# Optimization experiments

Hardware: AMD Instinct MI355X
Metric: run time of the kernel (lower is better)

The kernel has to match this reference:

```python
import jax, jax.numpy as jnp
import numpy as np

B, H, S = 128, 256, 19
K0, D0 = 512, 32
K1, D1 = 512, 64
K2, D2 = 512, 64


def _conv(x, w, b):
    # 3x3 SAME conv, NCHW / OIHW
    y = jax.lax.conv_general_dilated(x, w, (1, 1), 'SAME',
                                     dimension_numbers=('NCHW', 'OIHW', 'NCHW'))
    return y + b[None, :, None, None]


def _bn(x, g, b, eps=1e-5):
    # BatchNorm2d in training mode: batch statistics over (N, H, W)
    m = x.mean((0, 2, 3), keepdims=True)
    v = x.var((0, 2, 3), keepdims=True)
    return g[None, :, None, None] * (x - m) * jax.lax.rsqrt(v + eps) + b[None, :, None, None]


def _vq(lat, E):
    # cdist^2 -> argmin -> gather, with straight-through gradient copy
    shp = lat.shape
    d = E.shape[1]
    lp = lat.reshape(-1, d)                                   # row-major flatten, as torch .view
    dist = (lp * lp).sum(-1, keepdims=True) + (E * E).sum(-1) - 2.0 * (lp @ E.T)
    k = jnp.argmin(dist, axis=-1)
    zd = E[k]
    zg = lp + jax.lax.stop_gradient(zd - lp)
    return k.reshape(shp[0], -1), zd.reshape(shp), zg.reshape(shp)


def setup_inputs() -> dict:
    key = jax.random.key(0)
    ks = iter(jax.random.split(key, 64))
    def rn(shape, s=0.02):
        return (s * jax.random.normal(next(ks), shape)).astype(jnp.float32)
    inp = {
        'observations': jax.random.normal(next(ks), (B, 18, S, S), jnp.float32),
        'hierarchy_usages': jax.random.uniform(next(ks), (B, 2), jnp.float32),
        'h0_conv_w': rn((H, 18, 3, 3), 0.05), 'h0_conv_b': jnp.zeros((H,)),
        'h0_bn_g': jnp.ones((H,)), 'h0_bn_b': jnp.zeros((H,)),
        'rb_c1_w': rn((3, H, H, 3, 3)), 'rb_c1_b': jnp.zeros((3, H)),
        'rb_bn1_g': jnp.ones((3, H)), 'rb_bn1_b': jnp.zeros((3, H)),
        'rb_c2_w': rn((3, H, H, 3, 3)), 'rb_c2_b': jnp.zeros((3, H)),
        'rb_bn2_g': jnp.ones((3, H)), 'rb_bn2_b': jnp.zeros((3, H)),
        'h0_conv2_w': rn((32, H, 3, 3)), 'h0_conv2_b': jnp.zeros((32,)),
        'h0_bn2_g': jnp.ones((32,)), 'h0_bn2_b': jnp.zeros((32,)),
        'E0': rn((K0, D0)), 'E1': rn((K1, D1)), 'E2': rn((K2, D2)),
        'h1_fc_w': rn((D0 * S * S, 256)), 'h1_fc_b': jnp.zeros((256,)),
        'h1_fc2_w': rn((256, D1 * 8)), 'h1_fc2_b': jnp.zeros((D1 * 8,)),
        'h2_fc_w': rn((D1 * 8, 128)), 'h2_fc_b': jnp.zeros((128,)),
        'h2_fc2_w': rn((128, D2 * 8)), 'h2_fc2_b': jnp.zeros((D2 * 8,)),
        'h2_fc3_w': rn((D2 * 8, 128)), 'h2_fc3_b': jnp.zeros((128,)),
        'h2_fc4_w': rn((128, D1 * 8)), 'h2_fc4_b': jnp.zeros((D1 * 8,)),
        'h1_fc3_w': rn((D1 * 8, 256)), 'h1_fc3_b': jnp.zeros((256,)),
        'h1_fc4_w': rn((256, D0 * S * S)), 'h1_fc4_b': jnp.zeros((D0 * S * S,)),
        'policy_w': rn((32 * S * S, 362)), 'policy_b': jnp.zeros((362,)),
        'value_w': rn((32 * S * S, 1)), 'value_b': jnp.zeros((1,)),
    }
    return inp


def _forward(observations, hierarchy_usages, h0_conv_w, h0_conv_b, h0_bn_g, h0_bn_b,
             rb_c1_w, rb_c1_b, rb_bn1_g, rb_bn1_b, rb_c2_w, rb_c2_b, rb_bn2_g, rb_bn2_b,
             h0_conv2_w, h0_conv2_b, h0_bn2_g, h0_bn2_b, E0, E1, E2,
             h1_fc_w, h1_fc_b, h1_fc2_w, h1_fc2_b, h2_fc_w, h2_fc_b, h2_fc2_w, h2_fc2_b,
             h2_fc3_w, h2_fc3_b, h2_fc4_w, h2_fc4_b, h1_fc3_w, h1_fc3_b, h1_fc4_w, h1_fc4_b,
             policy_w, policy_b, value_w, value_b):
    n = observations.shape[0]
    x = jax.nn.relu(_bn(_conv(observations, h0_conv_w, h0_conv_b), h0_bn_g, h0_bn_b))
    for i in range(3):
        xi = x
        x = jax.nn.relu(_bn(_conv(x, rb_c1_w[i], rb_c1_b[i]), rb_bn1_g[i], rb_bn1_b[i]))
        x = _bn(_conv(x, rb_c2_w[i], rb_c2_b[i]), rb_bn2_g[i], rb_bn2_b[i])
        x = jax.nn.relu(xi + x)
    x = jnp.tanh(_bn(_conv(x, h0_conv2_w, h0_conv2_b), h0_bn2_g, h0_bn2_b))  # [B,32,19,19]
    ze0 = x
    k0, zq0, zql0 = _vq(x, E0)
    em0 = jnp.broadcast_to(E0.mean(0)[None, :, None, None], (n, E0.shape[1], S, S))
    x = jax.lax.stop_gradient(x).reshape(-1, 32 * S * S)
    x = jax.nn.relu(x @ h1_fc_w + h1_fc_b)
    x = jnp.tanh(x @ h1_fc2_w + h1_fc2_b).reshape(-1, E1.shape[1], 8)
    ze1 = x
    k1, zq1, zql1 = _vq(x, E1)
    em1 = jnp.broadcast_to(E1.mean(0)[None, :, None], (n, E1.shape[1], 8))
    x = jax.lax.stop_gradient(x).reshape(-1, E1.shape[1] * 8)
    x = jax.nn.relu(x @ h2_fc_w + h2_fc_b)
    x = jnp.tanh(x @ h2_fc2_w + h2_fc2_b).reshape(-1, E2.shape[1], 8)
    ze2 = x
    k2, zq2, zql2 = _vq(x, E2)
    em2 = jnp.broadcast_to(E2.mean(0)[None, :, None], (n, E2.shape[1], 8))
    # top-down decoder path
    x = zql2.reshape(-1, E2.shape[1] * 8)
    x = jax.nn.relu(x @ h2_fc3_w + h2_fc3_b)
    x = jnp.tanh(x @ h2_fc4_w + h2_fc4_b).reshape(-1, E1.shape[1], 8)
    u1 = hierarchy_usages[:, 1][:, None, None]
    x = u1 * zql1 + (1.0 - u1) * x
    x = x.reshape(-1, E1.shape[1] * 8)
    x = jax.nn.relu(x @ h1_fc3_w + h1_fc3_b)
    x = jnp.tanh(x @ h1_fc4_w + h1_fc4_b).reshape(-1, E0.shape[1], S, S)
    u0 = hierarchy_usages[:, 0][:, None, None, None]
    x = u0 * zql0 + (1.0 - u0) * x
    x = x.reshape(-1, 32 * S * S)
    policy = x @ policy_w + policy_b
    value = jnp.tanh(x @ value_w + value_b)
    return (policy, value, ze0, ze1, ze2, zq0, zq1, zq2, k0, k1, k2,
            zql0, zql1, zql2, em0, em1, em2)


def reference(observations, hierarchy_usages, h0_conv_w, h0_conv_b, h0_bn_g, h0_bn_b,
              rb_c1_w, rb_c1_b, rb_bn1_g, rb_bn1_b, rb_c2_w, rb_c2_b, rb_bn2_g, rb_bn2_b,
              h0_conv2_w, h0_conv2_b, h0_bn2_g, h0_bn2_b, E0, E1, E2,
              h1_fc_w, h1_fc_b, h1_fc2_w, h1_fc2_b, h2_fc_w, h2_fc_b, h2_fc2_w, h2_fc2_b,
              h2_fc3_w, h2_fc3_b, h2_fc4_w, h2_fc4_b, h1_fc3_w, h1_fc3_b, h1_fc4_w, h1_fc4_b,
              policy_w, policy_b, value_w, value_b):
    return _forward(observations, hierarchy_usages, h0_conv_w, h0_conv_b, h0_bn_g, h0_bn_b,
                    rb_c1_w, rb_c1_b, rb_bn1_g, rb_bn1_b, rb_c2_w, rb_c2_b, rb_bn2_g, rb_bn2_b,
                    h0_conv2_w, h0_conv2_b, h0_bn2_g, h0_bn2_b, E0, E1, E2,
                    h1_fc_w, h1_fc_b, h1_fc2_w, h1_fc2_b, h2_fc_w, h2_fc_b, h2_fc2_w, h2_fc2_b,
                    h2_fc3_w, h2_fc3_b, h2_fc4_w, h2_fc4_b, h1_fc3_w, h1_fc3_b, h1_fc4_w, h1_fc4_b,
                    policy_w, policy_b, value_w, value_b)
```

## Files before the change

kernel.cpp:

```cpp
#include <hip/hip_runtime.h>
#include <hip/hip_bf16.h>

typedef long long i64;
typedef __attribute__((ext_vector_type(8))) short bf16x8;
typedef __attribute__((ext_vector_type(4))) float f32x4;

static constexpr i64 OUT_POLICY = 0;
static constexpr i64 OUT_VALUE  = 46336;
static constexpr i64 OUT_ZE0    = 46464;
static constexpr i64 OUT_ZE1    = 1525120;
static constexpr i64 OUT_ZE2    = 1590656;
static constexpr i64 OUT_ZQ0    = 1656192;
static constexpr i64 OUT_ZQ1    = 3134848;
static constexpr i64 OUT_ZQ2    = 3200384;
static constexpr i64 OUT_K0     = 3265920;
static constexpr i64 OUT_K1     = 3312128;
static constexpr i64 OUT_K2     = 3313152;
static constexpr i64 OUT_ZQL0   = 3314176;
static constexpr i64 OUT_ZQL1   = 4792832;
static constexpr i64 OUT_ZQL2   = 4858368;
static constexpr i64 OUT_EM0    = 4923904;
static constexpr i64 OUT_EM1    = 6402560;
static constexpr i64 OUT_EM2    = 6468096;
static constexpr i64 OUT_TOTAL  = 6533632;

__device__ __forceinline__ short bf16_hi(float v, float* back)
{
    unsigned b = __float_as_uint(v);
    unsigned hb = (b + 0x8000u) & 0xFFFF0000u;
    *back = __uint_as_float(hb);
    return (short)(hb >> 16);
}
__device__ __forceinline__ short bf16_of(float v)
{
    return (short)((__float_as_uint(v) + 0x8000u) >> 16);
}

__global__ void wtr_k(const float* __restrict__ w, float* __restrict__ wt,
                      int COUT, int CIN)
{
    int total = COUT * CIN * 9;
    for (int idx = blockIdx.x * blockDim.x + threadIdx.x; idx < total;
         idx += gridDim.x * blockDim.x) {
        int co = idx / (CIN * 9);
        int r  = idx - co * CIN * 9;
        int ci = r / 9;
        int tap = r - ci * 9;
        wt[((i64)tap * CIN + ci) * COUT + co] = w[idx];
    }
}

__global__ void wtr4_k(const float* __restrict__ w, short* __restrict__ wt4,
                       int CIN, int COUT)
{
    int NC = CIN / 32;
    int total = NC * 9 * 2 * 8192;
    for (int idx = blockIdx.x * blockDim.x + threadIdx.x; idx < total;
         idx += gridDim.x * blockDim.x) {
        int tile = idx >> 13;
        int pos  = idx & 8191;
        int row   = pos >> 6;
        int sslot = (pos >> 3) & 7;
        int r     = pos & 7;
        int slot  = sslot ^ (row & 7);
        int k2    = slot * 8 + r;
        int ct = tile & 1;
        int s  = tile >> 1;
        int c  = s / 9, t = s - c * 9;
        int co = ct * 128 + row;
        int ci = c * 32 + (k2 & 31);
        short outv = 0;
        if (co < COUT) {
            float v = w[((i64)co * CIN + ci) * 9 + t];
            float hf;
            short hs = bf16_hi(v, &hf);
            outv = (k2 < 32) ? hs : bf16_of(v - hf);
        }
        wt4[idx] = outv;
    }
}

template<int CIN>
__global__ __launch_bounds__(256)
void convmfma_k(const float* __restrict__ X, const short* __restrict__ WT4,
                float* __restrict__ Y, int coutT)
{
    constexpr int NC = CIN / 32;
    constexpr int NS = NC * 9;
    __shared__ short Bt[2][8192];
    const int tid  = threadIdx.x;
    const int lane = tid & 63;
    const int w    = tid >> 6;
    const int wco  = (w & 1) * 64;
    const int wsp  = (w >> 1) * 64;
    const int col0 = blockIdx.x * 128;
    const int ct   = blockIdx.y;
    const int co0  = ct * 128;

    const int spS = tid & 127;
    const int cig = tid >> 7;
    const int colS = col0 + spS;
    const int nS = colS / 361;
    const int sS = colS - nS * 361;
    const int yS = sS / 19, xS = sS - yS * 19;
    const float* Xb = X + (i64)nS * CIN * 361 + sS;

    float xv[16];

#define B_LOAD(S)                                                               \
    {                                                                           \
        const int c_ = (S) / 9, t_ = (S) - c_ * 9;                              \
        const int ky_ = t_ / 3, kx_ = t_ - ky_ * 3;                             \
        const bool v_ = (yS + ky_ >= 1) & (yS + ky_ <= 19) &                    \
                        (xS + kx_ >= 1) & (xS + kx_ <= 19);                     \
        const float* xp_ = Xb + (i64)(c_ * 32 + cig * 16) * 361                 \
                              + (ky_ - 1) * 19 + (kx_ - 1);                     \
        _Pragma("unroll")                                                       \
        for (int j = 0; j < 16; j++) xv[j] = v_ ? xp_[(i64)j * 361] : 0.f;      \
    }

#define B_WRITE(BUF)                                                            \
    {                                                                           \
        bf16x8 h0, h1, l0, l1;                                                  \
        _Pragma("unroll")                                                       \
        for (int j = 0; j < 8; j++) {                                           \
            float hf;                                                           \
            short hs = bf16_hi(xv[j], &hf);                                     \
            h0[j] = hs; l0[j] = bf16_of(xv[j] - hf);                            \
        }                                                                       \
        _Pragma("unroll")                                                       \
        for (int j = 0; j < 8; j++) {                                           \
            float hf;                                                           \
            short hs = bf16_hi(xv[8 + j], &hf);                                 \
            h1[j] = hs; l1[j] = bf16_of(xv[8 + j] - hf);                        \
        }                                                                       \
        short* bp = &Bt[BUF][spS << 6];                                         \
        const int sw = spS & 7;                                                 \
        *(bf16x8*)(bp + (((cig * 2 + 0) ^ sw) << 3)) = h0;                      \
        *(bf16x8*)(bp + (((cig * 2 + 1) ^ sw) << 3)) = h1;                      \
        *(bf16x8*)(bp + (((4 + cig * 2 + 0) ^ sw) << 3)) = l0;                  \
        *(bf16x8*)(bp + (((4 + cig * 2 + 1) ^ sw) << 3)) = l1;                  \
    }

    f32x4 acc[4][4];
#pragma unroll
    for (int i = 0; i < 4; i++)
#pragma unroll
        for (int j = 0; j < 4; j++) acc[i][j] = (f32x4){0.f, 0.f, 0.f, 0.f};

    B_LOAD(0)
    B_WRITE(0)
    int cur = 0;
    for (int s = 0; s < NS; s++) {
        __syncthreads();
        if (s + 1 < NS) B_LOAD(s + 1)
        {
            const short* tb = WT4 + ((i64)(s * 2 + ct) << 13);
            bf16x8 afr[2][4];
#pragma unroll
            for (int ha = 0; ha < 2; ha++)
#pragma unroll
                for (int fa = 0; fa < 4; fa++) {
                    int row = wco + fa * 16 + (lane & 15);
                    int slot = ha * 4 + (lane >> 4);
                    afr[ha][fa] = *(const bf16x8*)(tb + (row << 6) + (((slot ^ (row & 7))) << 3));
                }
            bf16x8 bfr[2][4];
#pragma unroll
            for (int hb = 0; hb < 2; hb++)
#pragma unroll
                for (int fb = 0; fb < 4; fb++) {
                    int row = wsp + fb * 16 + (lane & 15);
                    int slot = hb * 4 + (lane >> 4);
                    bfr[hb][fb] = *(const bf16x8*)&Bt[cur][(row << 6) + (((slot ^ (row & 7))) << 3)];
                }
#pragma unroll
            for (int ha = 0; ha < 2; ha++)
#pragma unroll
                for (int fa = 0; fa < 4; fa++) {
                    bf16x8 af = afr[ha][fa];
#pragma unroll
                    for (int hb = 0; hb < 2; hb++)
#pragma unroll
                        for (int fb = 0; fb < 4; fb++)
                            acc[fa][fb] = __builtin_amdgcn_mfma_f32_16x16x32_bf16(
                                af, bfr[hb][fb], acc[fa][fb], 0, 0, 0);
                }
        }
        if (s + 1 < NS) B_WRITE(cur ^ 1)
        cur ^= 1;
    }
#undef B_LOAD
#undef B_WRITE

#pragma unroll
    for (int fb = 0; fb < 4; fb++) {
        int col = col0 + wsp + fb * 16 + (lane & 15);
        int nT = col / 361, sT = col - nT * 361;
        float* yp = Y + ((i64)nT * coutT + co0 + wco) * 361 + sT;
#pragma unroll
        for (int fa = 0; fa < 4; fa++)
#pragma unroll
            for (int r = 0; r < 4; r++) {
                int m = fa * 16 + (lane >> 4) * 4 + r;
                if (co0 + wco + m < coutT) yp[(i64)m * 361] = acc[fa][fb][r];
            }
    }
}

template<int CIN>
__global__ __launch_bounds__(256)
void convgemm_k(const float* __restrict__ X, const float* __restrict__ wt,
                float* __restrict__ Y, int wtW, int coW0, int coutT)
{
    constexpr int NCB = (CIN + 15) / 16;
    constexpr int NS  = 9 * NCB;
    __shared__ float Ws[2][16][128];
    __shared__ float Bs[2][16][128];
    const int tid  = threadIdx.x;
    const int col0 = blockIdx.x * 128;
    const int co0  = blockIdx.y * 128;
    const int tn = tid & 15;
    const int tm = (tid >> 4) & 15;
    const int kkS  = tid >> 5;
    const int cS0  = (tid & 31) * 4;

    int y_[4], x_[4];
    const float* Xb[4];
#pragma unroll
    for (int j = 0; j < 4; j++) {
        int colj = col0 + cS0 + j;
        int nj = colj / 361;
        int sj = colj - nj * 361;
        y_[j] = sj / 19;
        x_[j] = sj - y_[j] * 19;
        Xb[j] = X + ((i64)nj * CIN) * 361 + sj;
    }

    float4 wA, wB, bA, bB;

#define STAGE(S)                                                               \
    {                                                                          \
        const int tap_ = (S) / NCB, cb_ = ((S) % NCB) * 16;                    \
        const int ky_ = tap_ / 3, kx_ = tap_ - ky_ * 3;                        \
        const int doff_ = (ky_ - 1) * 19 + (kx_ - 1);                          \
        const int ci0_ = cb_ + kkS, ci1_ = ci0_ + 8;                           \
        const float* wr_ = wt + ((i64)(tap_ * CIN) + ci0_) * wtW               \
                              + coW0 + co0 + cS0;                              \
        const bool wok_ = (coW0 + co0 + cS0) < wtW;                            \
        wA = (wok_ && ci0_ < CIN) ? *(const float4*)wr_                        \
                                  : float4{0.f, 0.f, 0.f, 0.f};                \
        wB = (wok_ && ci1_ < CIN) ? *(const float4*)(wr_ + (i64)8 * wtW)       \
                                  : float4{0.f, 0.f, 0.f, 0.f};                \
        bool v0_ = (y_[0]+ky_>=1)&(y_[0]+ky_<=19)&(x_[0]+kx_>=1)&(x_[0]+kx_<=19); \
        bool v1_ = (y_[1]+ky_>=1)&(y_[1]+ky_<=19)&(x_[1]+kx_>=1)&(x_[1]+kx_<=19); \
        bool v2_ = (y_[2]+ky_>=1)&(y_[2]+ky_<=19)&(x_[2]+kx_>=1)&(x_[2]+kx_<=19); \
        bool v3_ = (y_[3]+ky_>=1)&(y_[3]+ky_<=19)&(x_[3]+kx_>=1)&(x_[3]+kx_<=19); \
        bA.x = (v0_ && ci0_ < CIN) ? Xb[0][(i64)ci0_ * 361 + doff_] : 0.f;     \
        bA.y = (v1_ && ci0_ < CIN) ? Xb[1][(i64)ci0_ * 361 + doff_] : 0.f;     \
        bA.z = (v2_ && ci0_ < CIN) ? Xb[2][(i64)ci0_ * 361 + doff_] : 0.f;     \
        bA.w = (v3_ && ci0_ < CIN) ? Xb[3][(i64)ci0_ * 361 + doff_] : 0.f;     \
        bB.x = (v0_ && ci1_ < CIN) ? Xb[0][(i64)ci1_ * 361 + doff_] : 0.f;     \
        bB.y = (v1_ && ci1_ < CIN) ? Xb[1][(i64)ci1_ * 361 + doff_] : 0.f;     \
        bB.z = (v2_ && ci1_ < CIN) ? Xb[2][(i64)ci1_ * 361 + doff_] : 0.f;     \
        bB.w = (v3_ && ci1_ < CIN) ? Xb[3][(i64)ci1_ * 361 + doff_] : 0.f;     \
    }

#define WRITE(BUF)                                                             \
    {                                                                          \
        *(float4*)&Ws[BUF][kkS    ][cS0] = wA;                                 \
        *(float4*)&Ws[BUF][kkS + 8][cS0] = wB;                                 \
        *(float4*)&Bs[BUF][kkS    ][cS0] = bA;                                 \
        *(float4*)&Bs[BUF][kkS + 8][cS0] = bB;                                 \
    }

    float acc[8][8];
#pragma unroll
    for (int i = 0; i < 8; i++)
#pragma unroll
        for (int j = 0; j < 8; j++) acc[i][j] = 0.f;

    STAGE(0)
    WRITE(0)
    int cur = 0;
    for (int s = 0; s < NS; s++) {
        __syncthreads();
        if (s + 1 < NS) STAGE(s + 1)
#pragma unroll
        for (int kk = 0; kk < 16; kk++) {
            const float4 w0 = *(const float4*)&Ws[cur][kk][tm * 4];
            const float4 w1 = *(const float4*)&Ws[cur][kk][tm * 4 + 64];
            const float4 b0 = *(const float4*)&Bs[cur][kk][tn * 4];
            const float4 b1 = *(const float4*)&Bs[cur][kk][tn * 4 + 64];
            float wv[8] = {w0.x, w0.y, w0.z, w0.w, w1.x, w1.y, w1.z, w1.w};
            float bv[8] = {b0.x, b0.y, b0.z, b0.w, b1.x, b1.y, b1.z, b1.w};
#pragma unroll
            for (int wi = 0; wi < 8; wi++)
#pragma unroll
                for (int bj = 0; bj < 8; bj++)
                    acc[wi][bj] = fmaf(wv[wi], bv[bj], acc[wi][bj]);
        }
        if (s + 1 < NS) WRITE(cur ^ 1)
        cur ^= 1;
    }
#undef STAGE
#undef WRITE

#pragma unroll
    for (int bj = 0; bj < 8; bj++) {
        int lc = (bj < 4) ? (tn * 4 + bj) : (64 + tn * 4 + bj - 4);
        int colT = col0 + lc;
        int nT = colT / 361;
        int sT = colT - nT * 361;
        float* yp = Y + ((i64)nT * coutT + co0) * 361 + sT;
#pragma unroll
        for (int wi = 0; wi < 8; wi++) {
            int co = (wi < 4) ? (tm * 4 + wi) : (64 + tm * 4 + wi - 4);
            if (co0 + co < coutT) yp[(i64)co * 361] = acc[wi][bj];
        }
    }
}

__global__ __launch_bounds__(256)
void bnstats_k(const float* __restrict__ x, const float* __restrict__ g,
               const float* __restrict__ b, float* __restrict__ scale,
               float* __restrict__ shift, int C)
{
    const int c = blockIdx.x;
    float s = 0.f, s2 = 0.f;
    for (int n = 0; n < 128; n++) {
        const float* p = x + ((i64)n * C + c) * 361;
        for (int i = threadIdx.x; i < 361; i += 256) {
            float v = p[i]; s += v; s2 += v * v;
        }
    }
    __shared__ float rs[4], rq[4];
    for (int o = 32; o > 0; o >>= 1) { s += __shfl_down(s, o); s2 += __shfl_down(s2, o); }
    int lane = threadIdx.x & 63, wid = threadIdx.x >> 6;
    if (lane == 0) { rs[wid] = s; rq[wid] = s2; }
    __syncthreads();
    if (threadIdx.x == 0) {
        float S = rs[0] + rs[1] + rs[2] + rs[3];
        float Q = rq[0] + rq[1] + rq[2] + rq[3];
        const float inv = 1.f / 46208.f;
        float m  = S * inv;
        float var = Q * inv - m * m;
        float sc = g[c] * rsqrtf(var + 1e-5f);
        scale[c] = sc;
        shift[c] = b[c] - m * sc;
    }
}

__global__ void bn_relu4_k(float4* __restrict__ x, const float* __restrict__ scale,
                           const float* __restrict__ shift, int C, int total4)
{
    for (int i = blockIdx.x * blockDim.x + threadIdx.x; i < total4; i += gridDim.x * blockDim.x) {
        float4 v = x[i];
        int e = i * 4;
        int c0 = (e / 361) % C, c1 = ((e + 1) / 361) % C;
        int c2 = ((e + 2) / 361) % C, c3 = ((e + 3) / 361) % C;
        v.x = fmaf(v.x, scale[c0], shift[c0]); v.x = v.x > 0.f ? v.x : 0.f;
        v.y = fmaf(v.y, scale[c1], shift[c1]); v.y = v.y > 0.f ? v.y : 0.f;
        v.z = fmaf(v.z, scale[c2], shift[c2]); v.z = v.z > 0.f ? v.z : 0.f;
        v.w = fmaf(v.w, scale[c3], shift[c3]); v.w = v.w > 0.f ? v.w : 0.f;
        x[i] = v;
    }
}

__global__ void bn_add_relu4_k(float4* __restrict__ xa, const float4* __restrict__ xc,
                               const float* __restrict__ scale, const float* __restrict__ shift,
                               int C, int total4)
{
    for (int i = blockIdx.x * blockDim.x + threadIdx.x; i < total4; i += gridDim.x * blockDim.x) {
        float4 a = xa[i], c = xc[i];
        int e = i * 4;
        int c0 = (e / 361) % C, c1 = ((e + 1) / 361) % C;
        int c2 = ((e + 2) / 361) % C, c3 = ((e + 3) / 361) % C;
        a.x += fmaf(c.x, scale[c0], shift[c0]); a.x = a.x > 0.f ? a.x : 0.f;
        a.y += fmaf(c.y, scale[c1], shift[c1]); a.y = a.y > 0.f ? a.y : 0.f;
        a.z += fmaf(c.z, scale[c2], shift[c2]); a.z = a.z > 0.f ? a.z : 0.f;
        a.w += fmaf(c.w, scale[c3], shift[c3]); a.w = a.w > 0.f ? a.w : 0.f;
        xa[i] = a;
    }
}

__global__ void bn_tanh_ws_k(const float* __restrict__ x, const float* __restrict__ scale,
                             const float* __restrict__ shift, float* __restrict__ zf, int total)
{
    for (int i = blockIdx.x * blockDim.x + threadIdx.x; i < total; i += gridDim.x * blockDim.x) {
        int c = (i / 361) & 31;
        zf[i] = tanhf(fmaf(x[i], scale[c], shift[c]));
    }
}

__global__ void prep_k(const float* __restrict__ E0, const float* __restrict__ E1,
                       const float* __restrict__ E2,
                       float* __restrict__ ee0, float* __restrict__ ee1, float* __restrict__ ee2,
                       float* __restrict__ cm0, float* __restrict__ cm1, float* __restrict__ cm2)
{
    int t = threadIdx.x;
    if (blockIdx.x == 0) {
        float s = 0.f; const float* e = E0 + (i64)t * 32;
        for (int d = 0; d < 32; d++) s += e[d] * e[d];
        ee0[t] = s;
    } else if (blockIdx.x == 1) {
        float s = 0.f; const float* e = E1 + (i64)t * 64;
        for (int d = 0; d < 64; d++) s += e[d] * e[d];
        ee1[t] = s;
    } else if (blockIdx.x == 2) {
        float s = 0.f; const float* e = E2 + (i64)t * 64;
        for (int d = 0; d < 64; d++) s += e[d] * e[d];
        ee2[t] = s;
    } else {
        if (t < 32) {
            float s = 0.f; for (int k = 0; k < 512; k++) s += E0[k * 32 + t];
            cm0[t] = s * (1.f / 512.f);
        } else if (t >= 64 && t < 128) {
            int d = t - 64; float s = 0.f; for (int k = 0; k < 512; k++) s += E1[k * 64 + d];
            cm1[d] = s * (1.f / 512.f);
        } else if (t >= 128 && t < 192) {
            int d = t - 128; float s = 0.f; for (int k = 0; k < 512; k++) s += E2[k * 64 + d];
            cm2[d] = s * (1.f / 512.f);
        }
    }
}

__global__ __launch_bounds__(256)
void vq0_k(const float* __restrict__ z, const float* __restrict__ E,
           const float* __restrict__ ee, float* __restrict__ zqf, int* __restrict__ ki)
{
    __shared__ float Es[256 * 32];
    int row = blockIdx.x * 256 + threadIdx.x;
    const bool live = row < 46208;
    const float* zp = z + (i64)(live ? row : 0) * 32;
    float zv[32]; float zz = 0.f;
#pragma unroll
    for (int d = 0; d < 32; d++) { float v = zp[d]; zv[d] = v; zz += v * v; }
    float best = 3.4e38f; int bk = 0;
    for (int h = 0; h < 2; h++) {
        __syncthreads();
        for (int i = threadIdx.x; i < 256 * 32; i += 256) Es[i] = E[h * 8192 + i];
        __syncthreads();
        for (int k = 0; k < 256; k++) {
            const float* e = Es + k * 32;
            float dot = 0.f;
#pragma unroll
            for (int d = 0; d < 32; d++) dot = fmaf(zv[d], e[d], dot);
            float dist = (zz + ee[h * 256 + k]) - 2.f * dot;
            if (dist < best) { best = dist; bk = h * 256 + k; }
        }
    }
    if (live) {
        ki[row] = bk;
        const float* eb = E + (i64)bk * 32;
#pragma unroll
        for (int d = 0; d < 32; d++) zqf[(i64)row * 32 + d] = eb[d];
    }
}

__global__ __launch_bounds__(256)
void vq64_k(const float* __restrict__ z, const float* __restrict__ E,
            const float* __restrict__ ee, float* __restrict__ zqf, int* __restrict__ ki)
{
    __shared__ float Es[128 * 64];
    int row = blockIdx.x * 256 + threadIdx.x;
    const float* zp = z + (i64)row * 64;
    float zv[64]; float zz = 0.f;
#pragma unroll
    for (int d = 0; d < 64; d++) { float v = zp[d]; zv[d] = v; zz += v * v; }
    float best = 3.4e38f; int bk = 0;
    for (int h = 0; h < 4; h++) {
        __syncthreads();
        for (int i = threadIdx.x; i < 128 * 64; i += 256) Es[i] = E[(i64)h * 8192 + i];
        __syncthreads();
        for (int k = 0; k < 128; k++) {
            const float* e = Es + k * 64;
            float dot = 0.f;
#pragma unroll
            for (int d = 0; d < 64; d++) dot = fmaf(zv[d], e[d], dot);
            float dist = (zz + ee[h * 128 + k]) - 2.f * dot;
            if (dist < best) { best = dist; bk = h * 128 + k; }
        }
    }
    ki[row] = bk;
    const float* eb = E + (i64)bk * 64;
#pragma unroll
    for (int d = 0; d < 64; d++) zqf[(i64)row * 64 + d] = eb[d];
}

__global__ __launch_bounds__(256)
void gemm_part_k(const float* __restrict__ A, const float* __restrict__ W,
                 float* __restrict__ part, int K, int N, int kchunk)
{
    __shared__ float As[128][17];
    __shared__ float Ws[16][64];
    const int n0 = blockIdx.x * 64;
    const int ks = blockIdx.y;
    const int kb0  = ks * kchunk;
    const int kend = min(K, kb0 + kchunk);
    const int tid = threadIdx.x;
    const int tn = tid & 15, tm = tid >> 4;
    float acc[8][4];
#pragma unroll
    for (int i = 0; i < 8; i++)
#pragma unroll
        for (int j = 0; j < 4; j++) acc[i][j] = 0.f;

    for (int kb = kb0; kb < kend; kb += 16) {
        __syncthreads();
        for (int i = tid; i < 2048; i += 256) {
            int m = i >> 4, kk = i & 15;
            int k = kb + kk;
            As[m][kk] = (k < kend) ? A[(i64)m * K + k] : 0.f;
        }
        for (int i = tid; i < 1024; i += 256) {
            int kk = i >> 6, nl = i & 63;
            int k = kb + kk, n = n0 + nl;
            Ws[kk][nl] = (k < kend && n < N) ? W[(i64)k * N + n] : 0.f;
        }
        __syncthreads();
#pragma unroll
        for (int kk = 0; kk < 16; kk++) {
            float av[8], wv[4];
#pragma unroll
            for (int i = 0; i < 8; i++) av[i] = As[tm * 8 + i][kk];
#pragma unroll
            for (int j = 0; j < 4; j++) wv[j] = Ws[kk][tn * 4 + j];
#pragma unroll
            for (int i = 0; i < 8; i++)
#pragma unroll
                for (int j = 0; j < 4; j++) acc[i][j] = fmaf(av[i], wv[j], acc[i][j]);
        }
    }
#pragma unroll
    for (int i = 0; i < 8; i++) {
        int m = tm * 8 + i;
#pragma unroll
        for (int j = 0; j < 4; j++) {
            int n = n0 + tn * 4 + j;
            if (n < N) part[((i64)ks * 128 + m) * N + n] = acc[i][j];
        }
    }
}

__global__ void combine_k(const float* __restrict__ part, const float* __restrict__ bias,
                          float* __restrict__ of, int MN, int N, int ksplit, int act)
{
    for (int i = blockIdx.x * blockDim.x + threadIdx.x; i < MN; i += gridDim.x * blockDim.x) {
        float s = 0.f;
        for (int t = 0; t < ksplit; t++) s += part[(i64)t * MN + i];
        s += bias[i % N];
        if (act == 1) s = s > 0.f ? s : 0.f;
        else if (act == 2) s = tanhf(s);
        of[i] = s;
    }
}

__global__ void blend_k(const float* __restrict__ q, const float* __restrict__ d,
                        const float* __restrict__ hu, int col, float* __restrict__ o,
                        int per_b, int total)
{
    for (int i = blockIdx.x * blockDim.x + threadIdx.x; i < total; i += gridDim.x * blockDim.x) {
        float u = hu[(i / per_b) * 2 + col];
        o[i] = u * q[i] + (1.f - u) * d[i];
    }
}

__global__ __launch_bounds__(256)
void value_k(const float* __restrict__ x, const float* __restrict__ w,
             const float* __restrict__ b, float* __restrict__ valf)
{
    int m = blockIdx.x;
    float s = 0.f;
    const float* xp = x + (i64)m * 11552;
    for (int k = threadIdx.x; k < 11552; k += 256) s = fmaf(xp[k], w[k], s);
    for (int o = 32; o > 0; o >>= 1) s += __shfl_down(s, o);
    __shared__ float r[4];
    int lane = threadIdx.x & 63, wid = threadIdx.x >> 6;
    if (lane == 0) r[wid] = s;
    __syncthreads();
    if (threadIdx.x == 0)
        valf[m] = tanhf(r[0] + r[1] + r[2] + r[3] + b[0]);
}

__global__ void emit_f32_k(const float* __restrict__ src, float* __restrict__ out, i64 off, int n)
{
    for (int i = blockIdx.x * blockDim.x + threadIdx.x; i < n; i += gridDim.x * blockDim.x)
        out[off + i] = src[i];
}

__global__ void emit_dup_k(const float* __restrict__ src, float* __restrict__ out,
                           i64 off1, i64 off2, int n)
{
    for (int i = blockIdx.x * blockDim.x + threadIdx.x; i < n; i += gridDim.x * blockDim.x) {
        float v = src[i];
        out[off1 + i] = v;
        out[off2 + i] = v;
    }
}

__global__ void emit_k_k(const int* __restrict__ ki, float* __restrict__ out, i64 off, int n)
{
    for (int i = blockIdx.x * blockDim.x + threadIdx.x; i < n; i += gridDim.x * blockDim.x)
        out[off + i] = (float)ki[i];
}

__global__ void emit_em_k(const float* __restrict__ cm, float* __restrict__ out, i64 off,
                          int D, int SPL, int total)
{
    for (int i = blockIdx.x * blockDim.x + threadIdx.x; i < total; i += gridDim.x * blockDim.x) {
        int c = (i / SPL) % D;
        out[off + i] = cm[c];
    }
}

__global__ void marker_k(float* __restrict__ out, int code)
{
    if (threadIdx.x < 64) out[threadIdx.x] = 3000.f + 100.f * code;
}

__global__ void sentinel_k(float* __restrict__ out)
{
    if (threadIdx.x < 128) out[OUT_VALUE + threadIdx.x] = 2000.0f;
}

extern "C" void kernel_launch(void* const* d_in, const int* in_sizes, int n_in,
                              void* d_out, int out_size, void* d_ws, size_t ws_size,
                              hipStream_t stream)
{
    float* out = (float*)d_out;

    int bad = -1;
    if (out_size != (int)OUT_TOTAL) bad = 0;
    else if (n_in != 41) bad = 1;
    else if (in_sizes[0] != 128 * 18 * 361) bad = 2;
    else if (in_sizes[21] != 11552 * 256) bad = 3;
    if (bad >= 0) { marker_k<<<1, 64, 0, stream>>>(out, bad); return; }

    const float* obs   = (const float*)d_in[0];
    const float* hier  = (const float*)d_in[1];
    const float* c0w   = (const float*)d_in[2];
    const float* bn0g  = (const float*)d_in[4];
    const float* bn0b  = (const float*)d_in[5];
    const float* rb1w  = (const float*)d_in[6];
    const float* rbn1g = (const float*)d_in[8];
    const float* rbn1b = (const float*)d_in[9];
    const float* rb2w  = (const float*)d_in[10];
    const float* rbn2g = (const float*)d_in[12];
    const float* rbn2b = (const float*)d_in[13];
    const float* c2w   = (const float*)d_in[14];
    const float* bn2g  = (const float*)d_in[16];
    const float* bn2b  = (const float*)d_in[17];
    const float* E0    = (const float*)d_in[18];
    const float* E1    = (const float*)d_in[19];
    const float* E2    = (const float*)d_in[20];
    const float* fc1w  = (const float*)d_in[21]; const float* fc1b  = (const float*)d_in[22];
    const float* fc2w  = (const float*)d_in[23]; const float* fc2b  = (const float*)d_in[24];
    const float* h2fw  = (const float*)d_in[25]; const float* h2fb  = (const float*)d_in[26];
    const float* h2f2w = (const float*)d_in[27]; const float* h2f2b = (const float*)d_in[28];
    const float* h2f3w = (const float*)d_in[29]; const float* h2f3b = (const float*)d_in[30];
    const float* h2f4w = (const float*)d_in[31]; const float* h2f4b = (const float*)d_in[32];
    const float* h1f3w = (const float*)d_in[33]; const float* h1f3b = (const float*)d_in[34];
    const float* h1f4w = (const float*)d_in[35]; const float* h1f4b = (const float*)d_in[36];
    const float* polw  = (const float*)d_in[37]; const float* polb  = (const float*)d_in[38];
    const float* valw  = (const float*)d_in[39]; const float* valb  = (const float*)d_in[40];

    float* wsf = (float*)d_ws;

    const size_t NEED_A = (size_t)36732928 * 4;
    const size_t NEED_C = (size_t)27860992 * 4;
    if (ws_size < NEED_C) {
        sentinel_k<<<1, 128, 0, stream>>>(out);
        return;
    }
    const bool fullC = (ws_size >= NEED_A);

    float* scale = wsf + 0;        float* shift = wsf + 256;
    float* ee0 = wsf + 512;        float* ee1 = wsf + 1024;   float* ee2 = wsf + 1536;
    float* cm0 = wsf + 2048;       float* cm1 = wsf + 2112;   float* cm2 = wsf + 2176;
    int*   k0i = (int*)(wsf + 4096);
    int*   k1i = (int*)(wsf + 50304);
    int*   k2i = (int*)(wsf + 51328);
    float* h1a  = wsf + 53248;
    float* ze1f = wsf + 86016;
    float* zq1f = wsf + 151552;
    float* h2a  = wsf + 217088;
    float* ze2f = wsf + 233472;
    float* zq2f = wsf + 299008;
    float* h2b  = wsf + 364544;
    float* decf = wsf + 380928;
    float* x1f  = wsf + 446464;
    float* h1b  = wsf + 512000;
    float* polf = wsf + 544768;
    float* valf = wsf + 591104;

    float* A    = wsf + 655360;
    float* B    = wsf + 12484608;
    float* C    = wsf + 24313856;
    float* WT   = fullC ? (wsf + 36143104) : (wsf + 27271168);
    float* ze0f = A;
    float* zq0f = wsf + 655360 + 1572864;
    float* dec0 = wsf + 655360 + 3145728;
    float* xf   = wsf + 655360 + 4718592;
    float* part = B;

    short* WT4 = (short*)d_out;

    const int TOT256 = 128 * 256 * 361;
    const int TOT32  = 128 * 32 * 361;
    const int TOT64  = 128 * 64 * 361;

    prep_k<<<4, 512, 0, stream>>>(E0, E1, E2, ee0, ee1, ee2, cm0, cm1, cm2);

    wtr_k<<<64, 256, 0, stream>>>(c0w, WT, 256, 18);
    convgemm_k<18><<<dim3(361, 2), 256, 0, stream>>>(obs, WT, A, 256, 0, 256);
    bnstats_k<<<256, 256, 0, stream>>>(A, bn0g, bn0b, scale, shift, 256);
    bn_relu4_k<<<1024, 256, 0, stream>>>((float4*)A, scale, shift, 256, TOT256 / 4);

    for (int i = 0; i < 3; i++) {
        if (fullC) {
            wtr4_k<<<1024, 256, 0, stream>>>(rb1w + (i64)i * 589824, WT4, 256, 256);
            convmfma_k<256><<<dim3(361, 2), 256, 0, stream>>>(A, WT4, B, 256);
        } else {
            wtr_k<<<576, 256, 0, stream>>>(rb1w + (i64)i * 589824, WT, 256, 256);
            convgemm_k<256><<<dim3(361, 2), 256, 0, stream>>>(A, WT, B, 256, 0, 256);
        }
        bnstats_k<<<256, 256, 0, stream>>>(B, rbn1g + i * 256, rbn1b + i * 256, scale, shift, 256);
        bn_relu4_k<<<1024, 256, 0, stream>>>((float4*)B, scale, shift, 256, TOT256 / 4);
        if (fullC) {
            wtr4_k<<<1024, 256, 0, stream>>>(rb2w + (i64)i * 589824, WT4, 256, 256);
            convmfma_k<256><<<dim3(361, 2), 256, 0, stream>>>(B, WT4, C, 256);
            bnstats_k<<<256, 256, 0, stream>>>(C, rbn2g + i * 256, rbn2b + i * 256, scale, shift, 256);
            bn_add_relu4_k<<<1024, 256, 0, stream>>>((float4*)A, (const float4*)C, scale, shift, 256, TOT256 / 4);
        } else {
            wtr_k<<<576, 256, 0, stream>>>(rb2w + (i64)i * 589824, WT, 256, 256);
            convgemm_k<256><<<dim3(361, 2), 256, 0, stream>>>(B, WT, C, 256, 0, 256);
            bnstats_k<<<256, 256, 0, stream>>>(C, rbn2g + i * 256, rbn2b + i * 256, scale, shift, 256);
            bn_add_relu4_k<<<1024, 256, 0, stream>>>((float4*)A, (const float4*)C, scale, shift, 256, TOT256 / 4);
        }
    }

    if (fullC) {
        wtr4_k<<<1024, 256, 0, stream>>>(c2w, WT4, 256, 32);
        convmfma_k<256><<<dim3(361, 1), 256, 0, stream>>>(A, WT4, C, 32);
    } else {
        wtr_k<<<72, 256, 0, stream>>>(c2w, WT, 32, 256);
        convgemm_k<256><<<dim3(361, 1), 256, 0, stream>>>(A, WT, C, 32, 0, 32);
    }
    bnstats_k<<<32, 256, 0, stream>>>(C, bn2g, bn2b, scale, shift, 32);
    bn_tanh_ws_k<<<1024, 256, 0, stream>>>(C, scale, shift, ze0f, TOT32);

    vq0_k<<<181, 256, 0, stream>>>(ze0f, E0, ee0, zq0f, k0i);

    gemm_part_k<<<dim3(4, 32), 256, 0, stream>>>(ze0f, fc1w, part, 11552, 256, 361);
    combine_k<<<128, 256, 0, stream>>>(part, fc1b, h1a, 128 * 256, 256, 32, 1);
    gemm_part_k<<<dim3(8, 4), 256, 0, stream>>>(h1a, fc2w, part, 256, 512, 64);
    combine_k<<<256, 256, 0, stream>>>(part, fc2b, ze1f, 128 * 512, 512, 4, 2);
    vq64_k<<<4, 256, 0, stream>>>(ze1f, E1, ee1, zq1f, k1i);

    gemm_part_k<<<dim3(2, 8), 256, 0, stream>>>(ze1f, h2fw, part, 512, 128, 64);
    combine_k<<<64, 256, 0, stream>>>(part, h2fb, h2a, 128 * 128, 128, 8, 1);
    gemm_part_k<<<dim3(8, 2), 256, 0, stream>>>(h2a, h2f2w, part, 128, 512, 64);
    combine_k<<<256, 256, 0, stream>>>(part, h2f2b, ze2f, 128 * 512, 512, 2, 2);
    vq64_k<<<4, 256, 0, stream>>>(ze2f, E2, ee2, zq2f, k2i);

    gemm_part_k<<<dim3(2, 8), 256, 0, stream>>>(zq2f, h2f3w, part, 512, 128, 64);
    combine_k<<<64, 256, 0, stream>>>(part, h2f3b, h2b, 128 * 128, 128, 8, 1);
    gemm_part_k<<<dim3(8, 2), 256, 0, stream>>>(h2b, h2f4w, part, 128, 512, 64);
    combine_k<<<256, 256, 0, stream>>>(part, h2f4b, decf, 128 * 512, 512, 2, 2);
    blend_k<<<256, 256, 0, stream>>>(zq1f, decf, hier, 1, x1f, 512, 65536);

    gemm_part_k<<<dim3(4, 8), 256, 0, stream>>>(x1f, h1f3w, part, 512, 256, 64);
    combine_k<<<128, 256, 0, stream>>>(part, h1f3b, h1b, 128 * 256, 256, 8, 1);
    gemm_part_k<<<dim3(181, 2), 256, 0, stream>>>(h1b, h1f4w, part, 256, 11552, 128);
    combine_k<<<1024, 256, 0, stream>>>(part, h1f4b, dec0, TOT32, 11552, 2, 2);
    blend_k<<<1024, 256, 0, stream>>>(zq0f, dec0, hier, 0, xf, 11552, TOT32);

    gemm_part_k<<<dim3(6, 16), 256, 0, stream>>>(xf, polw, part, 11552, 362, 722);
    combine_k<<<256, 256, 0, stream>>>(part, polb, polf, 128 * 362, 362, 16, 0);
    value_k<<<128, 256, 0, stream>>>(xf, valw, valb, valf);

    emit_f32_k<<<128, 256, 0, stream>>>(polf, out, OUT_POLICY, 46336);
    emit_f32_k<<<1, 128, 0, stream>>>(valf, out, OUT_VALUE, 128);
    emit_f32_k<<<1024, 256, 0, stream>>>(ze0f, out, OUT_ZE0, TOT32);
    emit_f32_k<<<256, 256, 0, stream>>>(ze1f, out, OUT_ZE1, 65536);
    emit_f32_k<<<256, 256, 0, stream>>>(ze2f, out, OUT_ZE2, 65536);
    emit_dup_k<<<1024, 256, 0, stream>>>(zq0f, out, OUT_ZQ0, OUT_ZQL0, TOT32);
    emit_dup_k<<<256, 256, 0, stream>>>(zq1f, out, OUT_ZQ1, OUT_ZQL1, 65536);
    emit_dup_k<<<256, 256, 0, stream>>>(zq2f, out, OUT_ZQ2, OUT_ZQL2, 65536);
    emit_k_k<<<181, 256, 0, stream>>>(k0i, out, OUT_K0, 46208);
    emit_k_k<<<4, 256, 0, stream>>>(k1i, out, OUT_K1, 1024);
    emit_k_k<<<4, 256, 0, stream>>>(k2i, out, OUT_K2, 1024);
    emit_em_k<<<1024, 256, 0, stream>>>(cm0, out, OUT_EM0, 32, 361, TOT32);
    emit_em_k<<<256, 256, 0, stream>>>(cm1, out, OUT_EM1, 64, 8, 65536);
    emit_em_k<<<256, 256, 0, stream>>>(cm2, out, OUT_EM2, 64, 8, 65536);
}
```

Baseline: 3.344 ms.

## Pre-split activations into swizzled bf16 hi/lo records fused with BN-ReLU for MFMA conv

Adds a tier that fuses BatchNorm+ReLU (and residual add) with splitting the activations into bf16 hi/lo pairs, stored in a per-pixel swizzled record layout. A new conv kernel loads these records straight into LDS via global_load_lds with a zero record for padding, so the conv no longer converts fp32 activations on the fly. It is meant to remove per-conv conversion and staging work and the separate BN-ReLU passes. The cost is a larger workspace, a path that only runs when the workspace is big enough, and extra record write traffic.

```diff
diff --git a/kernel.cpp b/kernel.cpp
--- a/kernel.cpp
+++ b/kernel.cpp
@@ -77,6 +77,164 @@
             outv = (k2 < 32) ? hs : bf16_of(v - hf);
         }
         wt4[idx] = outv;
+    }
+}
+
+template<int MODE>
+__global__ __launch_bounds__(256)
+void xsplit_k(const float* __restrict__ X, float* __restrict__ Aio,
+              const float* __restrict__ scale, const float* __restrict__ shift,
+              short* __restrict__ XS)
+{
+    int idx = blockIdx.x * 256 + threadIdx.x;
+    int g = idx % 46208;
+    int c = idx / 46208;
+    int n = g / 361;
+    int s = g - n * 361;
+    const i64 base = ((i64)n * 256 + c * 32) * 361 + s;
+
+    float vv[32];
+#pragma unroll
+    for (int j = 0; j < 32; j++) {
+        float x = X[base + (i64)j * 361];
+        float sc = scale[c * 32 + j], sh = shift[c * 32 + j];
+        float v;
+        if (MODE == 2) v = Aio[base + (i64)j * 361] + fmaf(x, sc, sh);
+        else           v = fmaf(x, sc, sh);
+        v = v > 0.f ? v : 0.f;
+        if (MODE >= 1) Aio[base + (i64)j * 361] = v;
+        vv[j] = v;
+    }
+    short hi[32], lo[32];
+#pragma unroll
+    for (int j = 0; j < 32; j++) {
+        float hf;
+        hi[j] = bf16_hi(vv[j], &hf);
+        lo[j] = bf16_of(vv[j] - hf);
+    }
+    short* rec = XS + ((i64)c * 46208 + g) * 64;
+    const int sw = g & 7;
+#pragma unroll
+    for (int l = 0; l < 8; l++) {
+        bf16x8 wv;
+#pragma unroll
+        for (int r = 0; r < 8; r++) {
+            int k2 = l * 8 + r;
+            int j = k2 & 31;
+            wv[r] = (k2 < 32) ? hi[j] : lo[j];
+        }
+        *(bf16x8*)(rec + ((l ^ sw) << 3)) = wv;
+    }
+}
+
+template<int CIN>
+__global__ __launch_bounds__(256)
+void convmfma_xs_k(const short* __restrict__ XS, const short* __restrict__ WT4,
+                   float* __restrict__ Y, int coutT, const short* __restrict__ zrec)
+{
+    constexpr int NC = CIN / 32;
+    constexpr int NS = NC * 9;
+    __shared__ short Bt[2][8192];
+    const int tid  = threadIdx.x;
+    const int lane = tid & 63;
+    const int w    = tid >> 6;
+    const int wco  = (w & 1) * 64;
+    const int wsp  = (w >> 1) * 64;
+    const int col0 = blockIdx.x * 128;
+    const int ct   = blockIdx.y;
+    const int co0  = ct * 128;
+
+    int gj[4], yj[4], xj[4], subj[4], cLj[4];
+#pragma unroll
+    for (int j = 0; j < 4; j++) {
+        int slotIdx = w * 256 + j * 64 + lane;
+        int colL = slotIdx >> 3;
+        subj[j] = slotIdx & 7;
+        cLj[j]  = colL;
+        gj[j] = col0 + colL;
+        int nn = gj[j] / 361;
+        int ss = gj[j] - nn * 361;
+        yj[j] = ss / 19;
+        xj[j] = ss - yj[j] * 19;
+    }
+
+#define BX_ISSUE(BUF, S)                                                        \
+    {                                                                           \
+        const int c_ = (S) / 9, t_ = (S) - c_ * 9;                              \
+        const int ky_ = t_ / 3, kx_ = t_ - ky_ * 3;                             \
+        const int doff_ = (ky_ - 1) * 19 + (kx_ - 1);                           \
+        _Pragma("unroll")                                                       \
+        for (int j = 0; j < 4; j++) {                                           \
+            bool v_ = (yj[j] + ky_ >= 1) & (yj[j] + ky_ <= 19) &                \
+                      (xj[j] + kx_ >= 1) & (xj[j] + kx_ <= 19);                 \
+            int adj_ = (cLj[j] & 7) ^ ((cLj[j] + doff_) & 7);                   \
+            const short* src = v_ ? (XS + ((i64)c_ * 46208 + (gj[j] + doff_)) * 64 \
+                                       + ((subj[j] ^ adj_) << 3))               \
+                                  : zrec;                                       \
+            __builtin_amdgcn_global_load_lds(src, &Bt[BUF][(w * 256 + j * 64) * 8], 16, 0, 0); \
+        }                                                                       \
+    }
+
+    f32x4 acc[4][4];
+#pragma unroll
+    for (int i = 0; i < 4; i++)
+#pragma unroll
+        for (int j = 0; j < 4; j++) acc[i][j] = (f32x4){0.f, 0.f, 0.f, 0.f};
+
+    BX_ISSUE(0, 0)
+    int cur = 0;
+    for (int s = 0; s < NS; s++) {
+        __syncthreads();
+        if (s + 1 < NS) BX_ISSUE(cur ^ 1, s + 1)
+        {
+            const short* tb = WT4 + ((i64)(s * 2 + ct) << 13);
+            bf16x8 afr[2][4];
+#pragma unroll
+            for (int ha = 0; ha < 2; ha++)
+#pragma unroll
+                for (int fa = 0; fa < 4; fa++) {
+                    int row = wco + fa * 16 + (lane & 15);
+                    int slot = ha * 4 + (lane >> 4);
+                    afr[ha][fa] = *(const bf16x8*)(tb + (row << 6) + (((slot ^ (row & 7))) << 3));
+                }
+            bf16x8 bfr[2][4];
+#pragma unroll
+            for (int hb = 0; hb < 2; hb++)
+#pragma unroll
+                for (int fb = 0; fb < 4; fb++) {
+                    int row = wsp + fb * 16 + (lane & 15);
+                    int slot = hb * 4 + (lane >> 4);
+                    bfr[hb][fb] = *(const bf16x8*)&Bt[cur][(row << 6) + (((slot ^ (row & 7))) << 3)];
+                }
+#pragma unroll
+            for (int ha = 0; ha < 2; ha++)
+#pragma unroll
+                for (int fa = 0; fa < 4; fa++) {
+                    bf16x8 af = afr[ha][fa];
+#pragma unroll
+                    for (int hb = 0; hb < 2; hb++)
+#pragma unroll
+                        for (int fb = 0; fb < 4; fb++)
+                            acc[fa][fb] = __builtin_amdgcn_mfma_f32_16x16x32_bf16(
+                                af, bfr[hb][fb], acc[fa][fb], 0, 0, 0);
+                }
+        }
+        cur ^= 1;
+    }
+#undef BX_ISSUE
+
+#pragma unroll
+    for (int fb = 0; fb < 4; fb++) {
+        int col = col0 + wsp + fb * 16 + (lane & 15);
+        int nT = col / 361, sT = col - nT * 361;
+        float* yp = Y + ((i64)nT * coutT + co0 + wco) * 361 + sT;
+#pragma unroll
+        for (int fa = 0; fa < 4; fa++)
+#pragma unroll
+            for (int r = 0; r < 4; r++) {
+                int m = fa * 16 + (lane >> 4) * 4 + r;
+                if (co0 + wco + m < coutT) yp[(i64)m * 361] = acc[fa][fb][r];
+            }
     }
 }
 
@@ -396,7 +554,8 @@
 __global__ void prep_k(const float* __restrict__ E0, const float* __restrict__ E1,
                        const float* __restrict__ E2,
                        float* __restrict__ ee0, float* __restrict__ ee1, float* __restrict__ ee2,
-                       float* __restrict__ cm0, float* __restrict__ cm1, float* __restrict__ cm2)
+                       float* __restrict__ cm0, float* __restrict__ cm1, float* __restrict__ cm2,
+                       float* __restrict__ wsf)
 {
     int t = threadIdx.x;
     if (blockIdx.x == 0) {
@@ -421,6 +580,8 @@
         } else if (t >= 128 && t < 192) {
             int d = t - 128; float s = 0.f; for (int k = 0; k < 512; k++) s += E2[k * 64 + d];
             cm2[d] = s * (1.f / 512.f);
+        } else if (t >= 192 && t < 224) {
+            wsf[2560 + (t - 192)] = 0.f;
         }
     }
 }
@@ -667,17 +828,19 @@
 
     float* wsf = (float*)d_ws;
 
+    const size_t NEED_X = (size_t)48562176 * 4;
     const size_t NEED_A = (size_t)36732928 * 4;
     const size_t NEED_C = (size_t)27860992 * 4;
     if (ws_size < NEED_C) {
         sentinel_k<<<1, 128, 0, stream>>>(out);
         return;
     }
-    const bool fullC = (ws_size >= NEED_A);
+    const int tier = (ws_size >= NEED_X) ? 2 : (ws_size >= NEED_A) ? 1 : 0;
 
     float* scale = wsf + 0;        float* shift = wsf + 256;
     float* ee0 = wsf + 512;        float* ee1 = wsf + 1024;   float* ee2 = wsf + 1536;
     float* cm0 = wsf + 2048;       float* cm1 = wsf + 2112;   float* cm2 = wsf + 2176;
+    const short* zrec = (const short*)(wsf + 2560);
     int*   k0i = (int*)(wsf + 4096);
     int*   k1i = (int*)(wsf + 50304);
     int*   k2i = (int*)(wsf + 51328);
@@ -694,61 +857,82 @@
     float* polf = wsf + 544768;
     float* valf = wsf + 591104;
 
-    float* A    = wsf + 655360;
-    float* B    = wsf + 12484608;
-    float* C    = wsf + 24313856;
-    float* WT   = fullC ? (wsf + 36143104) : (wsf + 27271168);
+    float* A   = wsf + 655360;
+    float* R   = wsf + 12484608;
+    float* C   = wsf + 24313856;
+    short* XSa = (short*)(wsf + 24313856);
+    short* XSb = (short*)(wsf + 36143104);
+    float* WT  = (tier == 2) ? (wsf + 47972352)
+               : (tier == 1) ? (wsf + 36143104) : (wsf + 27271168);
     float* ze0f = A;
     float* zq0f = wsf + 655360 + 1572864;
     float* dec0 = wsf + 655360 + 3145728;
     float* xf   = wsf + 655360 + 4718592;
-    float* part = B;
+    float* part = R;
 
     short* WT4 = (short*)d_out;
 
     const int TOT256 = 128 * 256 * 361;
     const int TOT32  = 128 * 32 * 361;
-    const int TOT64  = 128 * 64 * 361;
-
-    prep_k<<<4, 512, 0, stream>>>(E0, E1, E2, ee0, ee1, ee2, cm0, cm1, cm2);
+
+    prep_k<<<4, 512, 0, stream>>>(E0, E1, E2, ee0, ee1, ee2, cm0, cm1, cm2, wsf);
 
     wtr_k<<<64, 256, 0, stream>>>(c0w, WT, 256, 18);
-    convgemm_k<18><<<dim3(361, 2), 256, 0, stream>>>(obs, WT, A, 256, 0, 256);
-    bnstats_k<<<256, 256, 0, stream>>>(A, bn0g, bn0b, scale, shift, 256);
-    bn_relu4_k<<<1024, 256, 0, stream>>>((float4*)A, scale, shift, 256, TOT256 / 4);
-
-    for (int i = 0; i < 3; i++) {
-        if (fullC) {
+    if (tier == 2) {
+        convgemm_k<18><<<dim3(361, 2), 256, 0, stream>>>(obs, WT, R, 256, 0, 256);
+        bnstats_k<<<256, 256, 0, stream>>>(R, bn0g, bn0b, scale, shift, 256);
+        xsplit_k<1><<<1444, 256, 0, stream>>>(R, A, scale, shift, XSa);
+        for (int i = 0; i < 3; i++) {
             wtr4_k<<<1024, 256, 0, stream>>>(rb1w + (i64)i * 589824, WT4, 256, 256);
-            convmfma_k<256><<<dim3(361, 2), 256, 0, stream>>>(A, WT4, B, 256);
-        } else {
-            wtr_k<<<576, 256, 0, stream>>>(rb1w + (i64)i * 589824, WT, 256, 256);
-            convgemm_k<256><<<dim3(361, 2), 256, 0, stream>>>(A, WT, B, 256, 0, 256);
-        }
-        bnstats_k<<<256, 256, 0, stream>>>(B, rbn1g + i * 256, rbn1b + i * 256, scale, shift, 256);
-        bn_relu4_k<<<1024, 256, 0, stream>>>((float4*)B, scale, shift, 256, TOT256 / 4);
-        if (fullC) {
+            convmfma_xs_k<256><<<dim3(361, 2), 256, 0, stream>>>(XSa, WT4, R, 256, zrec);
+            bnstats_k<<<256, 256, 0, stream>>>(R, rbn1g + i * 256, rbn1b + i * 256, scale, shift, 256);
+            xsplit_k<0><<<1444, 256, 0, stream>>>(R, nullptr, scale, shift, XSb);
             wtr4_k<<<1024, 256, 0, stream>>>(rb2w + (i64)i * 589824, WT4, 256, 256);
-            convmfma_k<256><<<dim3(361, 2), 256, 0, stream>>>(B, WT4, C, 256);
+            convmfma_xs_k<256><<<dim3(361, 2), 256, 0, stream>>>(XSb, WT4, R, 256, zrec);
+            bnstats_k<<<256, 256, 0, stream>>>(R, rbn2g + i * 256, rbn2b + i * 256, scale, shift, 256);
+            xsplit_k<2><<<1444, 256, 0, stream>>>(R, A, scale, shift, XSa);
+        }
+        wtr4_k<<<1024, 256, 0, stream>>>(c2w, WT4, 256, 32);
+        convmfma_xs_k<256><<<dim3(361, 1), 256, 0, stream>>>(XSa, WT4, R, 32, zrec);
+        bnstats_k<<<32, 256, 0, stream>>>(R, bn2g, bn2b, scale, shift, 32);
+        bn_tanh_ws_k<<<1024, 256, 0, stream>>>(R, scale, shift, ze0f, TOT32);
+    } else if (tier == 1) {
+        convgemm_k<18><<<dim3(361, 2), 256, 0, stream>>>(obs, WT, A, 256, 0, 256);
+        bnstats_k<<<256, 256, 0, stream>>>(A, bn0g, bn0b, scale, shift, 256);
+        bn_relu4_k<<<1024, 256, 0, stream>>>((float4*)A, scale, shift, 256, TOT256 / 4);
+        for (int i = 0; i < 3; i++) {
+            wtr4_k<<<1024, 256, 0, stream>>>(rb1w + (i64)i * 589824, WT4, 256, 256);
+            convmfma_k<256><<<dim3(361, 2), 256, 0, stream>>>(A, WT4, R, 256);
+            bnstats_k<<<256, 256, 0, stream>>>(R, rbn1g + i * 256, rbn1b + i * 256, scale, shift, 256);
+            bn_relu4_k<<<1024, 256, 0, stream>>>((float4*)R, scale, shift, 256, TOT256 / 4);
+            wtr4_k<<<1024, 256, 0, stream>>>(rb2w + (i64)i * 589824, WT4, 256, 256);
+            convmfma_k<256><<<dim3(361, 2), 256, 0, stream>>>(R, WT4, C, 256);
             bnstats_k<<<256, 256, 0, stream>>>(C, rbn2g + i * 256, rbn2b + i * 256, scale, shift, 256);
             bn_add_relu4_k<<<1024, 256, 0, stream>>>((float4*)A, (const float4*)C, scale, shift, 256, TOT256 / 4);
-        } else {
+        }
+        wtr4_k<<<1024, 256, 0, stream>>>(c2w, WT4, 256, 32);
+        convmfma_k<256><<<dim3(361, 1), 256, 0, stream>>>(A, WT4, C, 32);
+        bnstats_k<<<32, 256, 0, stream>>>(C, bn2g, bn2b, scale, shift, 32);
+        bn_tanh_ws_k<<<1024, 256, 0, stream>>>(C, scale, shift, ze0f, TOT32);
+    } else {
+        convgemm_k<18><<<dim3(361, 2), 256, 0, stream>>>(obs, WT, A, 256, 0, 256);
+        bnstats_k<<<256, 256, 0, stream>>>(A, bn0g, bn0b, scale, shift, 256);
+        bn_relu4_k<<<1024, 256, 0, stream>>>((float4*)A, scale, shift, 256, TOT256 / 4);
+        for (int i = 0; i < 3; i++) {
+            wtr_k<<<576, 256, 0, stream>>>(rb1w + (i64)i * 589824, WT, 256, 256);
+            convgemm_k<256><<<dim3(361, 2), 256, 0, stream>>>(A, WT, R, 256, 0, 256);
+            bnstats_k<<<256, 256, 0, stream>>>(R, rbn1g + i * 256, rbn1b + i * 256, scale, shift, 256);
+            bn_relu4_k<<<1024, 256, 0, stream>>>((float4*)R, scale, shift, 256, TOT256 / 4);
             wtr_k<<<576, 256, 0, stream>>>(rb2w + (i64)i * 589824, WT, 256, 256);
-            convgemm_k<256><<<dim3(361, 2), 256, 0, stream>>>(B, WT, C, 256, 0, 256);
+            convgemm_k<256><<<dim3(361, 2), 256, 0, stream>>>(R, WT, C, 256, 0, 256);
             bnstats_k<<<256, 256, 0, stream>>>(C, rbn2g + i * 256, rbn2b + i * 256, scale, shift, 256);
             bn_add_relu4_k<<<1024, 256, 0, stream>>>((float4*)A, (const float4*)C, scale, shift, 256, TOT256 / 4);
         }
-    }
-
-    if (fullC) {
-        wtr4_k<<<1024, 256, 0, stream>>>(c2w, WT4, 256, 32);
-        convmfma_k<256><<<dim3(361, 1), 256, 0, stream>>>(A, WT4, C, 32);
-    } else {
         wtr_k<<<72, 256, 0, stream>>>(c2w, WT, 32, 256);
         convgemm_k<256><<<dim3(361, 1), 256, 0, stream>>>(A, WT, C, 32, 0, 32);
-    }
-    bnstats_k<<<32, 256, 0, stream>>>(C, bn2g, bn2b, scale, shift, 32);
-    bn_tanh_ws_k<<<1024, 256, 0, stream>>>(C, scale, shift, ze0f, TOT32);
+        bnstats_k<<<32, 256, 0, stream>>>(C, bn2g, bn2b, scale, shift, 32);
+        bn_tanh_ws_k<<<1024, 256, 0, stream>>>(C, scale, shift, ze0f, TOT32);
+    }
 
     vq0_k<<<181, 256, 0, stream>>>(ze0f, E0, ee0, zq0f, k0i);
 
```

After: 3.499 ms. 4.6% more time.
